# Kernel tuning notes

Hardware: AMD Instinct MI355X
Metric: run time of the kernel (lower is better)

Reference implementation:

```python
import jax, jax.numpy as jnp
import numpy as np

B, T, D, E, H, K = 4, 2048, 1024, 8, 2048, 2


def setup_inputs() -> dict:
    key = jax.random.key(0)
    k0, k1, k2, k3 = jax.random.split(key, 4)
    x = jax.random.normal(k0, (B, T, D), dtype=jnp.float32)
    router_w = jax.random.normal(k1, (E, D), dtype=jnp.float32) * (D ** -0.5)
    w1 = jax.random.normal(k2, (E, D, H), dtype=jnp.float32) * (D ** -0.5)
    w2 = jax.random.normal(k3, (E, H, D), dtype=jnp.float32) * (H ** -0.5)
    return {"x": x, "router_w": router_w, "w1": w1, "w2": w2}


def reference(x, router_w, w1, w2):
    Bb, Tt, Dd = x.shape
    N = Bb * Tt
    # --- router: top-k selection + renormalized softmax weights ---
    logits = jnp.einsum('btd,ed->bte', x, router_w)            # [B,T,E]
    top_vals, top_idx = jax.lax.top_k(logits, K)               # [B,T,K]
    top_w = jax.nn.softmax(top_vals, axis=-1)                  # [B,T,K]
    # --- dense per-expert FFN (relu-squared activation) ---
    xf = x.reshape(N, Dd)                                      # [N,D]
    h = jnp.einsum('nd,edh->enh', xf, w1)                      # [E,N,H]
    h = jnp.square(jax.nn.relu(h))
    y = jnp.einsum('enh,ehd->end', h, w2)                      # [E,N,D]
    # --- gather selected experts and combine ---
    idx_f = top_idx.reshape(N, K)                              # [N,K]
    w_f = top_w.reshape(N, K)                                  # [N,K]
    y_sel = y[idx_f, jnp.arange(N)[:, None]]                   # [N,K,D]
    out = jnp.einsum('nk,nkd->nd', w_f, y_sel)                 # [N,D]
    return out.reshape(Bb, Tt, Dd)
```

## Files before the change

### kernel.cpp

```cpp
#include <hip/hip_runtime.h>
#include <hip/hip_bf16.h>
#include <stdint.h>

#define ND    1024
#define NE    8
#define NH    2048
#define NTOK  8192
#define NPAIR (NTOK*2)

typedef unsigned short u16;
typedef __attribute__((ext_vector_type(8))) short bf16x8;
typedef __attribute__((ext_vector_type(4))) float f32x4;

__device__ __forceinline__ u16 f2bf(float f) {
    union { float f; unsigned u; } v; v.f = f;
    return (u16)((v.u + 0x7fffu + ((v.u >> 16) & 1u)) >> 16);
}

__device__ __forceinline__ void gl_lds16(const void* g, void* l) {
    __builtin_amdgcn_global_load_lds(
        (const __attribute__((address_space(1))) unsigned int*)g,
        (__attribute__((address_space(3))) unsigned int*)l, 16, 0, 0);
}

#define CTRL_OFFS  16
#define CTRL_BC    32
#define CTRL_BB    288
#define CTRL_TOPK  544

__global__ __launch_bounds__(256) void router_topk2(
    const float* __restrict__ x, const float* __restrict__ rw,
    int* __restrict__ topk_idx, float* __restrict__ topk_w)
{
    const int n    = blockIdx.x * 4 + (threadIdx.x >> 6);
    const int lane = threadIdx.x & 63;
    const float* xr = x + (size_t)n * ND;
    float4 xv[4];
    #pragma unroll
    for (int i = 0; i < 4; ++i) xv[i] = *(const float4*)(xr + lane*16 + i*4);

    float lg[NE];
    #pragma unroll
    for (int e = 0; e < NE; ++e) {
        const float* wr_ = rw + (size_t)e * ND + lane*16;
        float a = 0.f;
        #pragma unroll
        for (int i = 0; i < 4; ++i) {
            float4 wv = *(const float4*)(wr_ + i*4);
            a += xv[i].x*wv.x + xv[i].y*wv.y + xv[i].z*wv.z + xv[i].w*wv.w;
        }
        #pragma unroll
        for (int s = 32; s; s >>= 1) a += __shfl_xor(a, s);
        lg[e] = a;
    }
    if (lane == 0) {
        int i0 = 0; float v0 = lg[0];
        #pragma unroll
        for (int i = 1; i < NE; ++i) { float v = lg[i]; if (v > v0) { v0 = v; i0 = i; } }
        int i1 = -1; float v1 = -3.4e38f;
        #pragma unroll
        for (int i = 0; i < NE; ++i) {
            if (i == i0) continue;
            float v = lg[i]; if (v > v1) { v1 = v; i1 = i; }
        }
        float w0 = 1.f / (1.f + expf(v1 - v0));
        topk_idx[n*2]   = i0;  topk_idx[n*2+1] = i1;
        topk_w [n*2]    = w0;  topk_w [n*2+1]  = 1.f - w0;
    }
}

__global__ __launch_bounds__(256) void hist_blocks(
    const int* __restrict__ topk_idx, int* __restrict__ blockcounts)
{
    __shared__ int c[NE];
    const int tid = threadIdx.x;
    if (tid < NE) c[tid] = 0;
    __syncthreads();
    const int n = blockIdx.x * 256 + tid;
    atomicAdd(&c[topk_idx[n*2]],   1);
    atomicAdd(&c[topk_idx[n*2+1]], 1);
    __syncthreads();
    if (tid < NE) blockcounts[blockIdx.x * NE + tid] = c[tid];
}

__global__ void prefix2(int* __restrict__ ctrl)
{
    const int e = threadIdx.x;
    const int* bc = ctrl + CTRL_BC;
    int* offsets  = ctrl + CTRL_OFFS;
    int* bbase    = ctrl + CTRL_BB;
    if (e < NE) {
        int run = 0;
        int tmp[32];
        #pragma unroll
        for (int b = 0; b < 32; ++b) { tmp[b] = run; run += bc[b*NE + e]; }
        int total = run, pre = 0;
        #pragma unroll
        for (int i = 0; i < NE; ++i) {
            int v = __shfl(total, i);
            if (i < e) pre += v;
        }
        offsets[e] = pre;
        if (e == NE-1) offsets[NE] = pre + total;
        #pragma unroll
        for (int b = 0; b < 32; ++b) bbase[b*NE + e] = pre + tmp[b];
    }
}

__global__ __launch_bounds__(256) void scatter2(
    const int* __restrict__ topk_idx, const float* __restrict__ topk_w,
    const int* __restrict__ ctrl,
    int* __restrict__ bucket_tok, float* __restrict__ bucket_gw)
{
    __shared__ int wc[4][NE];
    const int b = blockIdx.x, tid = threadIdx.x;
    const int w = tid >> 6, l = tid & 63;
    const int n = b*256 + tid;
    const int e0 = topk_idx[n*2], e1 = topk_idx[n*2+1];
    const unsigned long long lt = (1ULL << l) - 1ULL;

    int rank0 = 0, rank1 = 0;
    #pragma unroll
    for (int e = 0; e < NE; ++e) {
        unsigned long long m0 = __ballot(e0 == e);
        unsigned long long m1 = __ballot(e1 == e);
        int c0 = __popcll(m0);
        if (e0 == e) rank0 = __popcll(m0 & lt);
        if (e1 == e) rank1 = c0 + __popcll(m1 & lt);
        if (l == 0) wc[w][e] = c0 + __popcll(m1);
    }
    __syncthreads();
    const int* bbase = ctrl + CTRL_BB;
    int wo0 = 0, wo1 = 0;
    #pragma unroll
    for (int w2 = 0; w2 < 4; ++w2) {
        if (w2 < w) { wo0 += wc[w2][e0]; wo1 += wc[w2][e1]; }
    }
    int p0 = bbase[b*NE + e0] + wo0 + rank0;
    int p1 = bbase[b*NE + e1] + wo1 + rank1;
    bucket_tok[p0] = n;  bucket_gw[p0] = topk_w[n*2];
    bucket_tok[p1] = n;  bucket_gw[p1] = topk_w[n*2+1];
}

__global__ __launch_bounds__(256) void transpose_cvt(
    const float* __restrict__ src, u16* __restrict__ dst, int R, int C)
{
    __shared__ float tb[64][65];
    const int tpc = C >> 6;
    const int tr = blockIdx.x / tpc;
    const int tc = blockIdx.x % tpc;
    src += (size_t)blockIdx.y * R * C;
    dst += (size_t)blockIdx.y * R * C;
    const int tid = threadIdx.x;
    #pragma unroll
    for (int i = 0; i < 4; ++i) {
        int idx = i*256 + tid;
        int r = idx >> 4, c4 = (idx & 15) * 4;
        float4 v = *(const float4*)(src + (size_t)(tr*64 + r)*C + tc*64 + c4);
        tb[r][c4] = v.x; tb[r][c4+1] = v.y; tb[r][c4+2] = v.z; tb[r][c4+3] = v.w;
    }
    __syncthreads();
    #pragma unroll
    for (int i = 0; i < 2; ++i) {
        int idx = i*256 + tid;
        int c = idx >> 3, s8 = (idx & 7) * 8;
        union { u16 u[8]; uint4 v; } pk;
        #pragma unroll
        for (int j = 0; j < 8; ++j) pk.u[j] = f2bf(tb[s8 + j][c]);
        *(uint4*)(dst + (size_t)(tc*64 + c)*R + tr*64 + s8) = pk.v;
    }
}

__global__ __launch_bounds__(256) void gather_cvt(
    const float* __restrict__ x, const int* __restrict__ bucket_tok, u16* __restrict__ Xg)
{
    const int pair = blockIdx.x * 4 + (threadIdx.x >> 6);
    const int lane = threadIdx.x & 63;
    const float* xr = x + (size_t)bucket_tok[pair] * ND;
    u16* dr = Xg + (size_t)pair * ND;
    const int d0 = lane * 16;
    float4 a = *(const float4*)(xr + d0);
    float4 b = *(const float4*)(xr + d0 + 4);
    float4 c = *(const float4*)(xr + d0 + 8);
    float4 d = *(const float4*)(xr + d0 + 12);
    union { u16 u[8]; uint4 v; } p0, p1;
    p0.u[0]=f2bf(a.x); p0.u[1]=f2bf(a.y); p0.u[2]=f2bf(a.z); p0.u[3]=f2bf(a.w);
    p0.u[4]=f2bf(b.x); p0.u[5]=f2bf(b.y); p0.u[6]=f2bf(b.z); p0.u[7]=f2bf(b.w);
    p1.u[0]=f2bf(c.x); p1.u[1]=f2bf(c.y); p1.u[2]=f2bf(c.z); p1.u[3]=f2bf(c.w);
    p1.u[4]=f2bf(d.x); p1.u[5]=f2bf(d.y); p1.u[6]=f2bf(d.z); p1.u[7]=f2bf(d.w);
    *(uint4*)(dr + d0)     = p0.v;
    *(uint4*)(dr + d0 + 8) = p1.v;
}

template<int KSTEPS, int EPI>
__global__ __launch_bounds__(256, 2) void pass_gemm(
    const u16* __restrict__ Amat, const u16* __restrict__ Bmat,
    const int* __restrict__ bucket_tok, const float* __restrict__ bucket_gw,
    const int* __restrict__ ctrl,
    u16* __restrict__ A1out, float* __restrict__ out)
{
    const int K   = KSTEPS * 64;
    const int e   = blockIdx.z;
    const int nt0 = blockIdx.x * 128;
    const int mt0 = blockIdx.y * 128;
    const int* offsets = ctrl + CTRL_OFFS;
    const int beg = offsets[e];
    const int cnt = offsets[e+1] - beg;
    if (mt0 >= cnt) return;

    extern __shared__ u16 sm[];

    const int tid  = threadIdx.x;
    const int wv   = tid >> 6;
    const int lane = tid & 63;
    const int l15  = lane & 15;
    const int grp  = lane >> 4;
    const int wr   = wv >> 1, wc = wv & 1;
    const int rmax = cnt - mt0 - 1;

    const u16* Abase = Amat + (size_t)beg * K;
    const u16* Bb    = Bmat + (size_t)e * NH * ND;

    const int rsub  = lane >> 3;
    const int csrc0 = lane & 7;

    auto stage = [&](int buf, int kt) {
        #pragma unroll
        for (int c = 0; c < 4; ++c) {
            int row = c*32 + wv*8 + rsub;
            int chunk = csrc0 ^ (row & 7);
            int lrow = row > rmax ? rmax : row;
            const u16* ga = Abase + (size_t)(mt0 + lrow) * K + kt*64 + chunk*8;
            gl_lds16(ga, sm + buf*8192 + c*2048 + wv*512);
            const u16* gb = Bb + (size_t)(nt0 + row) * K + kt*64 + chunk*8;
            gl_lds16(gb, sm + 16384 + buf*8192 + c*2048 + wv*512);
        }
    };

    f32x4 acc[4][4];
    #pragma unroll
    for (int mt = 0; mt < 4; ++mt)
        #pragma unroll
        for (int nt = 0; nt < 4; ++nt) acc[mt][nt] = 0;

    stage(0, 0);
    int cur = 0;
    for (int kt = 0; kt < KSTEPS; ++kt) {
        __syncthreads();
        if (kt + 1 < KSTEPS) stage(cur ^ 1, kt + 1);
        const char* As = (const char*)(sm + cur*8192);
        const char* Bs = (const char*)(sm + 16384 + cur*8192);
        #pragma unroll
        for (int kk = 0; kk < 2; ++kk) {
            bf16x8 af[4], bfr[4];
            #pragma unroll
            for (int mt = 0; mt < 4; ++mt) {
                int row = wr*64 + mt*16 + l15;
                int kb  = ((kk*32 + grp*8)*2) ^ ((row & 7) << 4);
                af[mt] = *(const bf16x8*)(As + row*128 + kb);
            }
            #pragma unroll
            for (int nt = 0; nt < 4; ++nt) {
                int row = wc*64 + nt*16 + l15;
                int kb  = ((kk*32 + grp*8)*2) ^ ((row & 7) << 4);
                bfr[nt] = *(const bf16x8*)(Bs + row*128 + kb);
            }
            #pragma unroll
            for (int mt = 0; mt < 4; ++mt)
                #pragma unroll
                for (int nt = 0; nt < 4; ++nt)
                    acc[mt][nt] = __builtin_amdgcn_mfma_f32_16x16x32_bf16(af[mt], bfr[nt], acc[mt][nt], 0,0,0);
        }
        cur ^= 1;
    }

    #pragma unroll
    for (int mt = 0; mt < 4; ++mt) {
        #pragma unroll
        for (int r = 0; r < 4; ++r) {
            int ml = mt0 + wr*64 + mt*16 + grp*4 + r;
            if (ml >= cnt) continue;
            if (EPI == 0) {
                u16* dst = A1out + (size_t)(beg + ml) * NH + nt0 + wc*64 + l15;
                #pragma unroll
                for (int nt = 0; nt < 4; ++nt) {
                    float v = fmaxf(acc[mt][nt][r], 0.f);
                    dst[nt*16] = f2bf(v * v);
                }
            } else {
                int   p = bucket_tok[beg + ml];
                float g = bucket_gw [beg + ml];
                float* orow = out + (size_t)p * ND + nt0 + wc*64 + l15;
                #pragma unroll
                for (int nt = 0; nt < 4; ++nt)
                    atomicAdd(orow + nt*16, g * acc[mt][nt][r]);
            }
        }
    }
}

#define TT 64
#define HC 128
#define XB_S 1032
#define AL_S 136
__global__ __launch_bounds__(512) void moe_mlp_mfma(
    const float* __restrict__ x, const u16* __restrict__ w1t, const u16* __restrict__ w2t,
    const int* __restrict__ bucket_tok, const float* __restrict__ bucket_gw,
    const int* __restrict__ ctrl, float* __restrict__ out)
{
    const int e = blockIdx.x;
    const int* offsets = ctrl + CTRL_OFFS;
    const int beg = offsets[e];
    const int cnt = offsets[e+1] - beg;
    const int tile = blockIdx.y;
    if (tile * TT >= cnt) return;

    extern __shared__ u16 smem_u[];
    u16* xb    = smem_u;
    u16* albuf = smem_u + 64 * XB_S;

    const int tid  = threadIdx.x;
    const int wv   = tid >> 6;
    const int lane = tid & 63;
    const int l15  = lane & 15;
    const int grp  = lane >> 4;
    const int kl   = grp * 8;

    {
        const int t = tid >> 3, part = tid & 7;
        int s = tile * TT + t;
        int bi = beg + (s < cnt ? s : cnt - 1);
        int p = bucket_tok[bi];
        const float* xr = x + (size_t)p * ND;
        #pragma unroll 4
        for (int i = 0; i < 32; ++i) {
            int d = part * 4 + i * 32;
            float4 xv = *(const float4*)(xr + d);
            ushort4 u4;
            u4.x = f2bf(xv.x); u4.y = f2bf(xv.y); u4.z = f2bf(xv.z); u4.w = f2bf(xv.w);
            *(ushort4*)&xb[t * XB_S + d] = u4;
        }
    }
    __syncthreads();

    const u16* w1t_e = w1t + (size_t)e * NH * ND;
    const u16* w2t_e = w2t + (size_t)e * ND * NH;
    const int dbase = wv * 128;

    f32x4 accY[8][4];
    #pragma unroll
    for (int dt = 0; dt < 8; ++dt)
        #pragma unroll
        for (int tt = 0; tt < 4; ++tt) accY[dt][tt] = 0;

    for (int hc = 0; hc < NH; hc += HC) {
        f32x4 c1[4];
        #pragma unroll
        for (int tt = 0; tt < 4; ++tt) c1[tt] = 0;
        const u16* ap = w1t_e + (size_t)(hc + wv*16 + l15) * ND + kl;
        for (int ks = 0; ks < 32; ++ks) {
            bf16x8 a = *(const bf16x8*)(ap + ks*32);
            #pragma unroll
            for (int tt = 0; tt < 4; ++tt) {
                bf16x8 b = *(const bf16x8*)&xb[(tt*16 + l15) * XB_S + ks*32 + kl];
                c1[tt] = __builtin_amdgcn_mfma_f32_16x16x32_bf16(a, b, c1[tt], 0,0,0);
            }
        }
        #pragma unroll
        for (int tt = 0; tt < 4; ++tt)
            #pragma unroll
            for (int r = 0; r < 4; ++r) {
                float v = fmaxf(c1[tt][r], 0.f);
                albuf[(tt*16 + l15) * AL_S + (wv*16 + grp*4 + r)] = f2bf(v * v);
            }
        __syncthreads();

        #pragma unroll
        for (int ks = 0; ks < 4; ++ks) {
            bf16x8 bb[4];
            #pragma unroll
            for (int tt = 0; tt < 4; ++tt)
                bb[tt] = *(const bf16x8*)&albuf[(tt*16 + l15) * AL_S + ks*32 + kl];
            const u16* w2p = w2t_e + (size_t)(dbase + l15) * NH + hc + ks*32 + kl;
            #pragma unroll
            for (int dt = 0; dt < 8; ++dt) {
                bf16x8 a = *(const bf16x8*)(w2p + (size_t)dt * 16 * NH);
                #pragma unroll
                for (int tt = 0; tt < 4; ++tt)
                    accY[dt][tt] = __builtin_amdgcn_mfma_f32_16x16x32_bf16(a, bb[tt], accY[dt][tt], 0,0,0);
            }
        }
        __syncthreads();
    }

    #pragma unroll
    for (int tt = 0; tt < 4; ++tt) {
        int s = tile * TT + tt*16 + l15;
        if (s >= cnt) continue;
        int p = bucket_tok[beg + s];
        float g = bucket_gw[beg + s];
        float* orow = out + (size_t)p * ND + dbase + grp*4;
        #pragma unroll
        for (int dt = 0; dt < 8; ++dt)
            #pragma unroll
            for (int r = 0; r < 4; ++r)
                atomicAdd(orow + dt*16 + r, g * accY[dt][tt][r]);
    }
}

extern "C" void kernel_launch(void* const* d_in, const int* in_sizes, int n_in,
                              void* d_out, int out_size, void* d_ws, size_t ws_size,
                              hipStream_t stream) {
    const float* x  = (const float*)d_in[0];
    const float* rw = (const float*)d_in[1];
    const float* w1 = (const float*)d_in[2];
    const float* w2 = (const float*)d_in[3];
    float* out = (float*)d_out;

    int*   ctrl        = (int*)d_ws;
    int*   blockcounts = ctrl + CTRL_BC;
    int*   topk_idx    = ctrl + CTRL_TOPK;
    float* topk_w      = (float*)(topk_idx + NPAIR);
    int*   bucket_tok  = (int*)(topk_w + NPAIR);
    float* bucket_gw   = (float*)(bucket_tok + NPAIR);

    const size_t CTRL_BYTES = (size_t)1 << 19;
    const size_t WT_BYTES   = (size_t)NE * NH * ND * sizeof(u16);
    const size_t A1_BYTES   = (size_t)NPAIR * NH * sizeof(u16);
    const size_t NEED1      = CTRL_BYTES + 2 * WT_BYTES;
    const size_t NEED2      = CTRL_BYTES + 2 * WT_BYTES + A1_BYTES;

    hipMemsetAsync(d_out, 0, (size_t)NTOK * ND * sizeof(float), stream);

    router_topk2<<<NTOK/4, 256, 0, stream>>>(x, rw, topk_idx, topk_w);
    hist_blocks<<<NTOK/256, 256, 0, stream>>>(topk_idx, blockcounts);
    prefix2<<<1, 64, 0, stream>>>(ctrl);
    scatter2<<<NTOK/256, 256, 0, stream>>>(topk_idx, topk_w, ctrl, bucket_tok, bucket_gw);

    if (ws_size >= NEED2) {
        u16* w1t = (u16*)((char*)d_ws + CTRL_BYTES);
        u16* shr = (u16*)((char*)d_ws + CTRL_BYTES + WT_BYTES);
        u16* A1  = (u16*)((char*)d_ws + CTRL_BYTES + 2*WT_BYTES);

        transpose_cvt<<<dim3(512, NE), 256, 0, stream>>>(w1, w1t, ND, NH);
        gather_cvt<<<NPAIR/4, 256, 0, stream>>>(x, bucket_tok, shr);

        pass_gemm<16, 0><<<dim3(NH/128, 128, NE), 256, 65536, stream>>>(
            shr, w1t, bucket_tok, bucket_gw, ctrl, A1, nullptr);

        transpose_cvt<<<dim3(512, NE), 256, 0, stream>>>(w2, shr, NH, ND);

        pass_gemm<32, 1><<<dim3(ND/128, 128, NE), 256, 65536, stream>>>(
            A1, shr, bucket_tok, bucket_gw, ctrl, nullptr, out);
    } else if (ws_size >= NEED1) {
        u16* w1t = (u16*)((char*)d_ws + CTRL_BYTES);
        u16* w2t = (u16*)((char*)d_ws + CTRL_BYTES + WT_BYTES);
        transpose_cvt<<<dim3(512, NE), 256, 0, stream>>>(w1, w1t, ND, NH);
        transpose_cvt<<<dim3(512, NE), 256, 0, stream>>>(w2, w2t, NH, ND);
        size_t shbytes = (size_t)(64 * XB_S + 64 * AL_S) * sizeof(u16);
        dim3 grid(NE, NPAIR / TT);
        moe_mlp_mfma<<<grid, 512, shbytes, stream>>>(x, w1t, w2t, bucket_tok, bucket_gw, ctrl, out);
    }
}
```

Baseline: 316.1 us.

## Enlarge grouped GEMM tiles to 256x256 with eight waves per block

The grouped expert GEMM kernel moves from 128x128 tiles with 4 waves to 256x256 tiles with 8 waves in a 2x4 layout. Each wave now computes 128x64 and loads A fragments one at a time inside the MFMA loop, doubling operand reuse per global/LDS load. The intent is to cut global and LDS traffic per FLOP. In exchange each block needs 128 KB of LDS and about 128 accumulator registers per thread, which lowers occupancy and grid size; with expert buckets of roughly 2048 rows the second GEMM may only have about one block per CU. The unused fused fallback kernel and the workspace-size branches are also removed.

```diff
diff --git a/kernel.cpp b/kernel.cpp
--- a/kernel.cpp
+++ b/kernel.cpp
@@ -193,7 +193,7 @@
 }
 
 template<int KSTEPS, int EPI>
-__global__ __launch_bounds__(256, 2) void pass_gemm(
+__global__ __launch_bounds__(512, 2) void pass_gemm(
     const u16* __restrict__ Amat, const u16* __restrict__ Bmat,
     const int* __restrict__ bucket_tok, const float* __restrict__ bucket_gw,
     const int* __restrict__ ctrl,
@@ -201,8 +201,8 @@
 {
     const int K   = KSTEPS * 64;
     const int e   = blockIdx.z;
-    const int nt0 = blockIdx.x * 128;
-    const int mt0 = blockIdx.y * 128;
+    const int nt0 = blockIdx.x * 256;
+    const int mt0 = blockIdx.y * 256;
     const int* offsets = ctrl + CTRL_OFFS;
     const int beg = offsets[e];
     const int cnt = offsets[e+1] - beg;
@@ -215,31 +215,32 @@
     const int lane = tid & 63;
     const int l15  = lane & 15;
     const int grp  = lane >> 4;
-    const int wr   = wv >> 1, wc = wv & 1;
+    const int wr   = wv >> 2;
+    const int wc   = wv & 3;
     const int rmax = cnt - mt0 - 1;
 
     const u16* Abase = Amat + (size_t)beg * K;
     const u16* Bb    = Bmat + (size_t)e * NH * ND;
 
-    const int rsub  = lane >> 3;
-    const int csrc0 = lane & 7;
+    const int rsub8 = lane >> 3;
+    const int cs    = lane & 7;
 
     auto stage = [&](int buf, int kt) {
         #pragma unroll
         for (int c = 0; c < 4; ++c) {
-            int row = c*32 + wv*8 + rsub;
-            int chunk = csrc0 ^ (row & 7);
-            int lrow = row > rmax ? rmax : row;
+            int row   = wv*32 + c*8 + rsub8;
+            int chunk = cs ^ (row & 7);
+            int lrow  = row > rmax ? rmax : row;
             const u16* ga = Abase + (size_t)(mt0 + lrow) * K + kt*64 + chunk*8;
-            gl_lds16(ga, sm + buf*8192 + c*2048 + wv*512);
+            gl_lds16(ga, sm + buf*16384 + wv*2048 + c*512);
             const u16* gb = Bb + (size_t)(nt0 + row) * K + kt*64 + chunk*8;
-            gl_lds16(gb, sm + 16384 + buf*8192 + c*2048 + wv*512);
+            gl_lds16(gb, sm + 32768 + buf*16384 + wv*2048 + c*512);
         }
     };
 
-    f32x4 acc[4][4];
-    #pragma unroll
-    for (int mt = 0; mt < 4; ++mt)
+    f32x4 acc[8][4];
+    #pragma unroll
+    for (int mt = 0; mt < 8; ++mt)
         #pragma unroll
         for (int nt = 0; nt < 4; ++nt) acc[mt][nt] = 0;
 
@@ -248,37 +249,35 @@
     for (int kt = 0; kt < KSTEPS; ++kt) {
         __syncthreads();
         if (kt + 1 < KSTEPS) stage(cur ^ 1, kt + 1);
-        const char* As = (const char*)(sm + cur*8192);
-        const char* Bs = (const char*)(sm + 16384 + cur*8192);
+        const char* As = (const char*)(sm + cur*16384);
+        const char* Bs = (const char*)(sm + 32768 + cur*16384);
         #pragma unroll
         for (int kk = 0; kk < 2; ++kk) {
-            bf16x8 af[4], bfr[4];
-            #pragma unroll
-            for (int mt = 0; mt < 4; ++mt) {
-                int row = wr*64 + mt*16 + l15;
-                int kb  = ((kk*32 + grp*8)*2) ^ ((row & 7) << 4);
-                af[mt] = *(const bf16x8*)(As + row*128 + kb);
-            }
+            bf16x8 bfr[4];
             #pragma unroll
             for (int nt = 0; nt < 4; ++nt) {
                 int row = wc*64 + nt*16 + l15;
-                int kb  = ((kk*32 + grp*8)*2) ^ ((row & 7) << 4);
+                int kb  = ((kk*4 + grp) ^ (row & 7)) << 4;
                 bfr[nt] = *(const bf16x8*)(Bs + row*128 + kb);
             }
             #pragma unroll
-            for (int mt = 0; mt < 4; ++mt)
+            for (int mt = 0; mt < 8; ++mt) {
+                int row = wr*128 + mt*16 + l15;
+                int kb  = ((kk*4 + grp) ^ (row & 7)) << 4;
+                bf16x8 af = *(const bf16x8*)(As + row*128 + kb);
                 #pragma unroll
                 for (int nt = 0; nt < 4; ++nt)
-                    acc[mt][nt] = __builtin_amdgcn_mfma_f32_16x16x32_bf16(af[mt], bfr[nt], acc[mt][nt], 0,0,0);
+                    acc[mt][nt] = __builtin_amdgcn_mfma_f32_16x16x32_bf16(af, bfr[nt], acc[mt][nt], 0,0,0);
+            }
         }
         cur ^= 1;
     }
 
     #pragma unroll
-    for (int mt = 0; mt < 4; ++mt) {
+    for (int mt = 0; mt < 8; ++mt) {
         #pragma unroll
         for (int r = 0; r < 4; ++r) {
-            int ml = mt0 + wr*64 + mt*16 + grp*4 + r;
+            int ml = mt0 + wr*128 + mt*16 + grp*4 + r;
             if (ml >= cnt) continue;
             if (EPI == 0) {
                 u16* dst = A1out + (size_t)(beg + ml) * NH + nt0 + wc*64 + l15;
@@ -299,115 +298,6 @@
     }
 }
 
-#define TT 64
-#define HC 128
-#define XB_S 1032
-#define AL_S 136
-__global__ __launch_bounds__(512) void moe_mlp_mfma(
-    const float* __restrict__ x, const u16* __restrict__ w1t, const u16* __restrict__ w2t,
-    const int* __restrict__ bucket_tok, const float* __restrict__ bucket_gw,
-    const int* __restrict__ ctrl, float* __restrict__ out)
-{
-    const int e = blockIdx.x;
-    const int* offsets = ctrl + CTRL_OFFS;
-    const int beg = offsets[e];
-    const int cnt = offsets[e+1] - beg;
-    const int tile = blockIdx.y;
-    if (tile * TT >= cnt) return;
-
-    extern __shared__ u16 smem_u[];
-    u16* xb    = smem_u;
-    u16* albuf = smem_u + 64 * XB_S;
-
-    const int tid  = threadIdx.x;
-    const int wv   = tid >> 6;
-    const int lane = tid & 63;
-    const int l15  = lane & 15;
-    const int grp  = lane >> 4;
-    const int kl   = grp * 8;
-
-    {
-        const int t = tid >> 3, part = tid & 7;
-        int s = tile * TT + t;
-        int bi = beg + (s < cnt ? s : cnt - 1);
-        int p = bucket_tok[bi];
-        const float* xr = x + (size_t)p * ND;
-        #pragma unroll 4
-        for (int i = 0; i < 32; ++i) {
-            int d = part * 4 + i * 32;
-            float4 xv = *(const float4*)(xr + d);
-            ushort4 u4;
-            u4.x = f2bf(xv.x); u4.y = f2bf(xv.y); u4.z = f2bf(xv.z); u4.w = f2bf(xv.w);
-            *(ushort4*)&xb[t * XB_S + d] = u4;
-        }
-    }
-    __syncthreads();
-
-    const u16* w1t_e = w1t + (size_t)e * NH * ND;
-    const u16* w2t_e = w2t + (size_t)e * ND * NH;
-    const int dbase = wv * 128;
-
-    f32x4 accY[8][4];
-    #pragma unroll
-    for (int dt = 0; dt < 8; ++dt)
-        #pragma unroll
-        for (int tt = 0; tt < 4; ++tt) accY[dt][tt] = 0;
-
-    for (int hc = 0; hc < NH; hc += HC) {
-        f32x4 c1[4];
-        #pragma unroll
-        for (int tt = 0; tt < 4; ++tt) c1[tt] = 0;
-        const u16* ap = w1t_e + (size_t)(hc + wv*16 + l15) * ND + kl;
-        for (int ks = 0; ks < 32; ++ks) {
-            bf16x8 a = *(const bf16x8*)(ap + ks*32);
-            #pragma unroll
-            for (int tt = 0; tt < 4; ++tt) {
-                bf16x8 b = *(const bf16x8*)&xb[(tt*16 + l15) * XB_S + ks*32 + kl];
-                c1[tt] = __builtin_amdgcn_mfma_f32_16x16x32_bf16(a, b, c1[tt], 0,0,0);
-            }
-        }
-        #pragma unroll
-        for (int tt = 0; tt < 4; ++tt)
-            #pragma unroll
-            for (int r = 0; r < 4; ++r) {
-                float v = fmaxf(c1[tt][r], 0.f);
-                albuf[(tt*16 + l15) * AL_S + (wv*16 + grp*4 + r)] = f2bf(v * v);
-            }
-        __syncthreads();
-
-        #pragma unroll
-        for (int ks = 0; ks < 4; ++ks) {
-            bf16x8 bb[4];
-            #pragma unroll
-            for (int tt = 0; tt < 4; ++tt)
-                bb[tt] = *(const bf16x8*)&albuf[(tt*16 + l15) * AL_S + ks*32 + kl];
-            const u16* w2p = w2t_e + (size_t)(dbase + l15) * NH + hc + ks*32 + kl;
-            #pragma unroll
-            for (int dt = 0; dt < 8; ++dt) {
-                bf16x8 a = *(const bf16x8*)(w2p + (size_t)dt * 16 * NH);
-                #pragma unroll
-                for (int tt = 0; tt < 4; ++tt)
-                    accY[dt][tt] = __builtin_amdgcn_mfma_f32_16x16x32_bf16(a, bb[tt], accY[dt][tt], 0,0,0);
-            }
-        }
-        __syncthreads();
-    }
-
-    #pragma unroll
-    for (int tt = 0; tt < 4; ++tt) {
-        int s = tile * TT + tt*16 + l15;
-        if (s >= cnt) continue;
-        int p = bucket_tok[beg + s];
-        float g = bucket_gw[beg + s];
-        float* orow = out + (size_t)p * ND + dbase + grp*4;
-        #pragma unroll
-        for (int dt = 0; dt < 8; ++dt)
-            #pragma unroll
-            for (int r = 0; r < 4; ++r)
-                atomicAdd(orow + dt*16 + r, g * accY[dt][tt][r]);
-    }
-}
-
 extern "C" void kernel_launch(void* const* d_in, const int* in_sizes, int n_in,
                               void* d_out, int out_size, void* d_ws, size_t ws_size,
                               hipStream_t stream) {
@@ -427,8 +317,6 @@
     const size_t CTRL_BYTES = (size_t)1 << 19;
     const size_t WT_BYTES   = (size_t)NE * NH * ND * sizeof(u16);
     const size_t A1_BYTES   = (size_t)NPAIR * NH * sizeof(u16);
-    const size_t NEED1      = CTRL_BYTES + 2 * WT_BYTES;
-    const size_t NEED2      = CTRL_BYTES + 2 * WT_BYTES + A1_BYTES;
 
     hipMemsetAsync(d_out, 0, (size_t)NTOK * ND * sizeof(float), stream);
 
@@ -437,28 +325,18 @@
     prefix2<<<1, 64, 0, stream>>>(ctrl);
     scatter2<<<NTOK/256, 256, 0, stream>>>(topk_idx, topk_w, ctrl, bucket_tok, bucket_gw);
 
-    if (ws_size >= NEED2) {
-        u16* w1t = (u16*)((char*)d_ws + CTRL_BYTES);
-        u16* shr = (u16*)((char*)d_ws + CTRL_BYTES + WT_BYTES);
-        u16* A1  = (u16*)((char*)d_ws + CTRL_BYTES + 2*WT_BYTES);
-
-        transpose_cvt<<<dim3(512, NE), 256, 0, stream>>>(w1, w1t, ND, NH);
-        gather_cvt<<<NPAIR/4, 256, 0, stream>>>(x, bucket_tok, shr);
-
-        pass_gemm<16, 0><<<dim3(NH/128, 128, NE), 256, 65536, stream>>>(
-            shr, w1t, bucket_tok, bucket_gw, ctrl, A1, nullptr);
-
-        transpose_cvt<<<dim3(512, NE), 256, 0, stream>>>(w2, shr, NH, ND);
-
-        pass_gemm<32, 1><<<dim3(ND/128, 128, NE), 256, 65536, stream>>>(
-            A1, shr, bucket_tok, bucket_gw, ctrl, nullptr, out);
-    } else if (ws_size >= NEED1) {
-        u16* w1t = (u16*)((char*)d_ws + CTRL_BYTES);
-        u16* w2t = (u16*)((char*)d_ws + CTRL_BYTES + WT_BYTES);
-        transpose_cvt<<<dim3(512, NE), 256, 0, stream>>>(w1, w1t, ND, NH);
-        transpose_cvt<<<dim3(512, NE), 256, 0, stream>>>(w2, w2t, NH, ND);
-        size_t shbytes = (size_t)(64 * XB_S + 64 * AL_S) * sizeof(u16);
-        dim3 grid(NE, NPAIR / TT);
-        moe_mlp_mfma<<<grid, 512, shbytes, stream>>>(x, w1t, w2t, bucket_tok, bucket_gw, ctrl, out);
-    }
-}
+    u16* w1t = (u16*)((char*)d_ws + CTRL_BYTES);
+    u16* shr = (u16*)((char*)d_ws + CTRL_BYTES + WT_BYTES);
+    u16* A1  = (u16*)((char*)d_ws + CTRL_BYTES + 2*WT_BYTES);
+
+    transpose_cvt<<<dim3(512, NE), 256, 0, stream>>>(w1, w1t, ND, NH);
+    gather_cvt<<<NPAIR/4, 256, 0, stream>>>(x, bucket_tok, shr);
+
+    pass_gemm<16, 0><<<dim3(NH/256, NPAIR/256, NE), 512, 131072, stream>>>(
+        shr, w1t, bucket_tok, bucket_gw, ctrl, A1, nullptr);
+
+    transpose_cvt<<<dim3(512, NE), 256, 0, stream>>>(w2, shr, NH, ND);
+
+    pass_gemm<32, 1><<<dim3(ND/256, NPAIR/256, NE), 512, 131072, stream>>>(
+        A1, shr, bucket_tok, bucket_gw, ctrl, nullptr, out);
+}
```

Result: slower. 324.3 us (+2.6%).
